# Performance work log

Hardware: AMD Instinct MI355X
Metric: run time of the kernel (lower is better)

The kernel has to match this reference:

```python
import jax, jax.numpy as jnp
import numpy as np

B, T, IN, H, OUT, L = 64, 4096, 32, 128, 32, 2


def setup_inputs() -> dict:
    key = jax.random.key(0)
    ks = jax.random.split(key, 12)
    s = 1.0 / np.sqrt(H)
    inp = {"x": jax.random.normal(ks[0], (B, T, IN), dtype=jnp.float32)}
    # layer 0 (input_dim -> H), layer 1 (H -> H); PyTorch GRU layout: [3H, in] with gates (r, z, n)
    inp["W_ih0"] = jax.random.uniform(ks[1], (3 * H, IN), jnp.float32, -s, s)
    inp["W_hh0"] = jax.random.uniform(ks[2], (3 * H, H), jnp.float32, -s, s)
    inp["b_ih0"] = jax.random.uniform(ks[3], (3 * H,), jnp.float32, -s, s)
    inp["b_hh0"] = jax.random.uniform(ks[4], (3 * H,), jnp.float32, -s, s)
    inp["W_ih1"] = jax.random.uniform(ks[5], (3 * H, H), jnp.float32, -s, s)
    inp["W_hh1"] = jax.random.uniform(ks[6], (3 * H, H), jnp.float32, -s, s)
    inp["b_ih1"] = jax.random.uniform(ks[7], (3 * H,), jnp.float32, -s, s)
    inp["b_hh1"] = jax.random.uniform(ks[8], (3 * H,), jnp.float32, -s, s)
    inp["fc_w"] = jax.random.uniform(ks[9], (OUT, H), jnp.float32, -s, s)
    inp["fc_b"] = jax.random.uniform(ks[10], (OUT,), jnp.float32, -s, s)
    return inp


def _gru_layer(x_seq, W_ih, W_hh, b_ih, b_hh):
    # x_seq: [B, T, in]; precompute the input projection as one big GEMM
    gi = jnp.einsum("bti,gi->btg", x_seq, W_ih) + b_ih  # [B, T, 3H]
    h0 = jnp.zeros((x_seq.shape[0], W_hh.shape[1]), x_seq.dtype)

    def step(h, gi_t):
        gh = h @ W_hh.T + b_hh  # [B, 3H]
        i_r, i_z, i_n = jnp.split(gi_t, 3, axis=-1)
        h_r, h_z, h_n = jnp.split(gh, 3, axis=-1)
        r = jax.nn.sigmoid(i_r + h_r)
        z = jax.nn.sigmoid(i_z + h_z)
        n = jnp.tanh(i_n + r * h_n)
        h_new = (1.0 - z) * n + z * h
        return h_new, h_new

    hT, outs = jax.lax.scan(step, h0, jnp.swapaxes(gi, 0, 1))  # outs: [T, B, H]
    return jnp.swapaxes(outs, 0, 1), hT


def reference(x, W_ih0, W_hh0, b_ih0, b_hh0, W_ih1, W_hh1, b_ih1, b_hh1, fc_w, fc_b):
    y0, h0 = _gru_layer(x, W_ih0, W_hh0, b_ih0, b_hh0)
    y1, h1 = _gru_layer(y0, W_ih1, W_hh1, b_ih1, b_hh1)
    out = jnp.einsum("bth,oh->bto", y1, fc_w) + fc_b  # [B, T, OUT]
    h = jnp.stack([h0, h1], axis=0)  # [n_layers, B, H]
    return out, h
```

## Files before the change

kernel.cpp:

```cpp
#include <hip/hip_runtime.h>

#define BB 64
#define TT 4096
#define IN0 32
#define HH 128
#define NOUT 32

typedef _Float16 h2 __attribute__((ext_vector_type(2)));
typedef _Float16 h8v __attribute__((ext_vector_type(8)));
typedef float f32x4 __attribute__((ext_vector_type(4)));
union H8 { h8v v; h2 p[4]; };

struct SM {
    alignas(16) _Float16 hf0[2][HH];
    alignas(16) _Float16 hf1[2][HH];
    alignas(16) _Float16 xh[2][16][IN0];
    alignas(16) float    pfc[2][NOUT * 20];
    alignas(16) float    outbuf[32][NOUT];
};

__device__ __forceinline__ float fast_sigmoid(float x) {
    x = fminf(fmaxf(x, -30.f), 30.f);
    float e = __expf(-x);
    return __builtin_amdgcn_rcpf(1.f + e);
}
__device__ __forceinline__ float fast_tanh(float x) {
    x = fminf(fmaxf(x, -15.f), 15.f);
    float e = __expf(-2.f * x);
    return (1.f - e) * __builtin_amdgcn_rcpf(1.f + e);
}
__device__ __forceinline__ float fdot2(h2 a, h2 b, float c) {
#if __has_builtin(__builtin_amdgcn_fdot2)
    return __builtin_amdgcn_fdot2(a, b, c, false);
#else
    return fmaf((float)a.x, (float)b.x, fmaf((float)a.y, (float)b.y, c));
#endif
}
__device__ __forceinline__ h2 cvt2(float a, float b) {
    h2 r; r.x = (_Float16)a; r.y = (_Float16)b; return r;
}
__device__ __forceinline__ f32x4 MF(h8v a, h8v b, f32x4 c) {
    return __builtin_amdgcn_mfma_f32_16x16x32_f16(a, b, c, 0, 0, 0);
}

extern "C" __global__ __launch_bounds__(512)
__attribute__((amdgpu_waves_per_eu(2, 2)))
void gru_mfma_kernel(
    const float* __restrict__ x,
    const float* __restrict__ W_ih0, const float* __restrict__ W_hh0,
    const float* __restrict__ b_ih0, const float* __restrict__ b_hh0,
    const float* __restrict__ W_ih1, const float* __restrict__ W_hh1,
    const float* __restrict__ b_ih1, const float* __restrict__ b_hh1,
    const float* __restrict__ fc_w, const float* __restrict__ fc_b,
    float* __restrict__ out, float* __restrict__ hstack)
{
    __shared__ SM sm;
    const int b = blockIdx.x;
    const int tid = threadIdx.x;
    const int w = tid >> 6;
    const int l = tid & 63;
    const int ln = l & 15;
    const int kg = (l >> 4) * 8;
    const int jw = 16 * w + ln;
    const int o = tid & 31, ks = tid >> 5;
    const float* xb = x + (size_t)b * TT * IN0;
    float* outb = out + (size_t)b * TT * NOUT;
    float* hstack_l0 = hstack + (size_t)b * HH;
    float* hstack_l1 = hstack + (size_t)(BB + b) * HH;

    auto LDB = [&](const float* W, int ldk, int row, int kb) -> h8v {
        const float* p = W + (size_t)row * ldk + kb + kg;
        float4 f0 = *(const float4*)p;
        float4 f1 = *(const float4*)(p + 4);
        H8 u;
        u.p[0] = cvt2(f0.x, f0.y); u.p[1] = cvt2(f0.z, f0.w);
        u.p[2] = cvt2(f1.x, f1.y); u.p[3] = cvt2(f1.z, f1.w);
        return u.v;
    };
    h8v Br1i[4], Br1h[4], Bz1i[4], Bz1h[4], Bn1i[4], Bn1h[4];
    h8v Br0[4], Bz0[4], Bh0[4];
    #pragma unroll
    for (int c = 0; c < 4; ++c) {
        Br1i[c] = LDB(W_ih1, HH, jw,       32 * c);
        Bz1i[c] = LDB(W_ih1, HH, jw + 128, 32 * c);
        Bn1i[c] = LDB(W_ih1, HH, jw + 256, 32 * c);
        Br1h[c] = LDB(W_hh1, HH, jw,       32 * c);
        Bz1h[c] = LDB(W_hh1, HH, jw + 128, 32 * c);
        Bn1h[c] = LDB(W_hh1, HH, jw + 256, 32 * c);
        Br0[c]  = LDB(W_hh0, HH, jw,       32 * c);
        Bz0[c]  = LDB(W_hh0, HH, jw + 128, 32 * c);
        Bh0[c]  = LDB(W_hh0, HH, jw + 256, 32 * c);
    }
    const h8v Br0x = LDB(W_ih0, IN0, jw,       0);
    const h8v Bz0x = LDB(W_ih0, IN0, jw + 128, 0);
    const h8v Bn0x = LDB(W_ih0, IN0, jw + 256, 0);

    const float bvr1 = b_ih1[jw] + b_hh1[jw];
    const float bvz1 = b_ih1[jw + 128] + b_hh1[jw + 128];
    const float bvi1 = b_ih1[jw + 256];
    const float bvh1 = b_hh1[jw + 256];
    const float bvr0 = b_ih0[jw] + b_hh0[jw];
    const float bvz0 = b_ih0[jw + 128] + b_hh0[jw + 128];
    const float bvi0 = b_ih0[jw + 256];
    const float bvh0 = b_hh0[jw + 256];
    h2 wfc[4];
    #pragma unroll
    for (int m = 0; m < 4; ++m) {
        float2 f = *(const float2*)&fc_w[(size_t)o * HH + ks * 8 + 2 * m];
        wfc[m] = cvt2(f.x, f.y);
    }
    const float fcbr = fc_b[o];
    const f32x4 z4 = {0.f, 0.f, 0.f, 0.f};

    if (tid < HH) {
        sm.hf0[0][tid] = (_Float16)0.f; sm.hf0[1][tid] = (_Float16)0.f;
        sm.hf1[0][tid] = (_Float16)0.f; sm.hf1[1][tid] = (_Float16)0.f;
    }
    if (tid < 128) {
        float4 f = ((const float4*)xb)[tid];
        ((h2*)&sm.xh[0][0][0])[2 * tid]     = cvt2(f.x, f.y);
        ((h2*)&sm.xh[0][0][0])[2 * tid + 1] = cvt2(f.z, f.w);
    }
    __syncthreads();

    float hp0 = 0.f, hp1 = 0.f;
    float4 pf;
    for (int s = 0; s <= TT + 4; ++s) {
        const int cur = s & 1, nxt = cur ^ 1;
        if (tid < 128 && (s & 15) == 0 && s + 16 < TT)
            pf = ((const float4*)(xb + (size_t)(s + 16) * IN0))[tid];
        if (tid >= 128 && tid < 256 && (s & 15) == 4 && s >= 20 && (s >> 4) <= 256) {
            const int k = tid - 128;
            const int fb = ((s >> 4) - 1) * 16;
            const int t = fb + (k >> 3);
            float4 v = *(const float4*)&sm.outbuf[t & 31][(k & 7) * 4];
            *(float4*)&outb[(size_t)t * NOUT + (k & 7) * 4] = v;
        }
        const _Float16* h0b = &sm.hf0[cur][0] + kg;
        const _Float16* h1b = &sm.hf1[cur][0] + kg;
        const _Float16* xr  = &sm.xh[(s >> 4) & 1][s & 15][0] + kg;
        h8v a0 = *(const h8v*)(h0b);
        h8v a1 = *(const h8v*)(h1b);
        f32x4 r1  = MF(a0, Br1i[0], z4); r1 = MF(a1, Br1h[0], r1);
        f32x4 zz1 = MF(a0, Bz1i[0], z4); zz1 = MF(a1, Bz1h[0], zz1);
        f32x4 n1i = MF(a0, Bn1i[0], z4);
        f32x4 n1h = MF(a1, Bn1h[0], z4);
        f32x4 r0  = MF(a0, Br0[0], z4);
        f32x4 zz0 = MF(a0, Bz0[0], z4);
        f32x4 n0h = MF(a0, Bh0[0], z4);
        #pragma unroll
        for (int c = 1; c < 4; ++c) {
            a0 = *(const h8v*)(h0b + 32 * c);
            a1 = *(const h8v*)(h1b + 32 * c);
            r1  = MF(a0, Br1i[c], r1);  r1  = MF(a1, Br1h[c], r1);
            zz1 = MF(a0, Bz1i[c], zz1); zz1 = MF(a1, Bz1h[c], zz1);
            n1i = MF(a0, Bn1i[c], n1i);
            n1h = MF(a1, Bn1h[c], n1h);
            r0  = MF(a0, Br0[c], r0);
            zz0 = MF(a0, Bz0[c], zz0);
            n0h = MF(a0, Bh0[c], n0h);
        }
        h8v ax = *(const h8v*)xr;
        r0  = MF(ax, Br0x, r0);
        zz0 = MF(ax, Bz0x, zz0);
        f32x4 n0i = MF(ax, Bn0x, z4);

        {
            float rg = fast_sigmoid(r0.x + bvr0);
            float zg = fast_sigmoid(zz0.x + bvz0);
            float ng = fast_tanh(n0i.x + bvi0 + rg * (n0h.x + bvh0));
            float hn = (1.f - zg) * ng + zg * hp0;
            if (s <= TT - 1) {
                hp0 = hn;
                if (l < 16) {
                    sm.hf0[nxt][jw] = (_Float16)hn;
                    if (s == TT - 1) hstack_l0[jw] = hn;
                }
            }
        }
        {
            float rg = fast_sigmoid(r1.x + bvr1);
            float zg = fast_sigmoid(zz1.x + bvz1);
            float ng = fast_tanh(n1i.x + bvi1 + rg * (n1h.x + bvh1));
            float hn = (1.f - zg) * ng + zg * hp1;
            if (s >= 1 && s <= TT) {
                hp1 = hn;
                if (l < 16) {
                    sm.hf1[nxt][jw] = (_Float16)hn;
                    if (s == TT) hstack_l1[jw] = hn;
                }
            }
        }
        if (s >= 2 && s <= TT + 1) {
            H8 hv; hv.v = *(const h8v*)&sm.hf1[cur][ks * 8];
            float ssum = 0.f;
            #pragma unroll
            for (int m = 0; m < 4; ++m) ssum = fdot2(wfc[m], hv.p[m], ssum);
            sm.pfc[cur][o * 20 + ks] = ssum;
        }
        if (s >= 3 && s <= TT + 2 && tid < NOUT) {
            float ssum = fcbr;
            #pragma unroll
            for (int m = 0; m < 4; ++m) {
                float4 v = *(const float4*)&sm.pfc[nxt][tid * 20 + 4 * m];
                ssum += v.x + v.y + v.z + v.w;
            }
            sm.outbuf[(s - 3) & 31][tid] = ssum;
        }
        if (tid < 128 && (s & 15) == 8 && s + 8 < TT) {
            const int buf = ((s >> 4) + 1) & 1;
            ((h2*)&sm.xh[buf][0][0])[2 * tid]     = cvt2(pf.x, pf.y);
            ((h2*)&sm.xh[buf][0][0])[2 * tid + 1] = cvt2(pf.z, pf.w);
        }
        __syncthreads();
    }
}

extern "C" void kernel_launch(void* const* d_in, const int* in_sizes, int n_in,
                              void* d_out, int out_size, void* d_ws, size_t ws_size,
                              hipStream_t stream) {
    const float* x     = (const float*)d_in[0];
    const float* W_ih0 = (const float*)d_in[1];
    const float* W_hh0 = (const float*)d_in[2];
    const float* b_ih0 = (const float*)d_in[3];
    const float* b_hh0 = (const float*)d_in[4];
    const float* W_ih1 = (const float*)d_in[5];
    const float* W_hh1 = (const float*)d_in[6];
    const float* b_ih1 = (const float*)d_in[7];
    const float* b_hh1 = (const float*)d_in[8];
    const float* fc_w  = (const float*)d_in[9];
    const float* fc_b  = (const float*)d_in[10];

    float* out    = (float*)d_out;
    float* hstack = out + (size_t)BB * TT * NOUT;

    gru_mfma_kernel<<<BB, 512, 0, stream>>>(
        x, W_ih0, W_hh0, b_ih0, b_hh0,
        W_ih1, W_hh1, b_ih1, b_hh1,
        fc_w, fc_b, out, hstack);
}
```

Measured before the change: 4.330 ms.

## Compute FC projection with MFMA and unroll time loop by two

Replaces the per-thread fdot2 FC partial sums (16 partials per output) with one MFMA per wave over a 32-wide K chunk, cutting the reduction to 4 partials per output. All h-vector LDS loads are hoisted ahead of the MFMA chain, and the time loop is unrolled by two so the double-buffer index is a compile-time constant. This shortens the serial per-step critical path at the cost of extra registers for the preloaded operands and the FC weight fragment. The loop runs to TT+5 iterations in pairs, so one extra step executes, but the existing guards keep it harmless.

```diff
diff --git a/kernel.cpp b/kernel.cpp
--- a/kernel.cpp
+++ b/kernel.cpp
@@ -28,13 +28,6 @@
     x = fminf(fmaxf(x, -15.f), 15.f);
     float e = __expf(-2.f * x);
     return (1.f - e) * __builtin_amdgcn_rcpf(1.f + e);
-}
-__device__ __forceinline__ float fdot2(h2 a, h2 b, float c) {
-#if __has_builtin(__builtin_amdgcn_fdot2)
-    return __builtin_amdgcn_fdot2(a, b, c, false);
-#else
-    return fmaf((float)a.x, (float)b.x, fmaf((float)a.y, (float)b.y, c));
-#endif
 }
 __device__ __forceinline__ h2 cvt2(float a, float b) {
     h2 r; r.x = (_Float16)a; r.y = (_Float16)b; return r;
@@ -62,7 +55,9 @@
     const int ln = l & 15;
     const int kg = (l >> 4) * 8;
     const int jw = 16 * w + ln;
-    const int o = tid & 31, ks = tid >> 5;
+    const int ofc = 16 * (w & 1) + ln;
+    const int cfc = w >> 1;
+    const int fco = kg + 32 * cfc;
     const float* xb = x + (size_t)b * TT * IN0;
     float* outb = out + (size_t)b * TT * NOUT;
     float* hstack_l0 = hstack + (size_t)b * HH;
@@ -94,6 +89,7 @@
     const h8v Br0x = LDB(W_ih0, IN0, jw,       0);
     const h8v Bz0x = LDB(W_ih0, IN0, jw + 128, 0);
     const h8v Bn0x = LDB(W_ih0, IN0, jw + 256, 0);
+    const h8v Bfc  = LDB(fc_w,  HH,  ofc,      32 * cfc);
 
     const float bvr1 = b_ih1[jw] + b_hh1[jw];
     const float bvz1 = b_ih1[jw + 128] + b_hh1[jw + 128];
@@ -103,13 +99,7 @@
     const float bvz0 = b_ih0[jw + 128] + b_hh0[jw + 128];
     const float bvi0 = b_ih0[jw + 256];
     const float bvh0 = b_hh0[jw + 256];
-    h2 wfc[4];
-    #pragma unroll
-    for (int m = 0; m < 4; ++m) {
-        float2 f = *(const float2*)&fc_w[(size_t)o * HH + ks * 8 + 2 * m];
-        wfc[m] = cvt2(f.x, f.y);
-    }
-    const float fcbr = fc_b[o];
+    const float fcbr = (tid < NOUT) ? fc_b[tid] : 0.f;
     const f32x4 z4 = {0.f, 0.f, 0.f, 0.f};
 
     if (tid < HH) {
@@ -125,8 +115,9 @@
 
     float hp0 = 0.f, hp1 = 0.f;
     float4 pf;
-    for (int s = 0; s <= TT + 4; ++s) {
-        const int cur = s & 1, nxt = cur ^ 1;
+
+    auto body = [&](int s, int cur) {
+        const int nxt = cur ^ 1;
         if (tid < 128 && (s & 15) == 0 && s + 16 < TT)
             pf = ((const float4*)(xb + (size_t)(s + 16) * IN0))[tid];
         if (tid >= 128 && tid < 256 && (s & 15) == 4 && s >= 20 && (s >> 4) <= 256) {
@@ -138,29 +129,32 @@
         }
         const _Float16* h0b = &sm.hf0[cur][0] + kg;
         const _Float16* h1b = &sm.hf1[cur][0] + kg;
-        const _Float16* xr  = &sm.xh[(s >> 4) & 1][s & 15][0] + kg;
-        h8v a0 = *(const h8v*)(h0b);
-        h8v a1 = *(const h8v*)(h1b);
-        f32x4 r1  = MF(a0, Br1i[0], z4); r1 = MF(a1, Br1h[0], r1);
-        f32x4 zz1 = MF(a0, Bz1i[0], z4); zz1 = MF(a1, Bz1h[0], zz1);
-        f32x4 n1i = MF(a0, Bn1i[0], z4);
-        f32x4 n1h = MF(a1, Bn1h[0], z4);
-        f32x4 r0  = MF(a0, Br0[0], z4);
-        f32x4 zz0 = MF(a0, Bz0[0], z4);
-        f32x4 n0h = MF(a0, Bh0[0], z4);
+        h8v a0[4], a1[4];
+        #pragma unroll
+        for (int c = 0; c < 4; ++c) {
+            a0[c] = *(const h8v*)(h0b + 32 * c);
+            a1[c] = *(const h8v*)(h1b + 32 * c);
+        }
+        h8v ax  = *(const h8v*)(&sm.xh[(s >> 4) & 1][s & 15][0] + kg);
+        h8v afc = *(const h8v*)(&sm.hf1[cur][0] + fco);
+        f32x4 r1  = MF(a0[0], Br1i[0], z4); r1  = MF(a1[0], Br1h[0], r1);
+        f32x4 zz1 = MF(a0[0], Bz1i[0], z4); zz1 = MF(a1[0], Bz1h[0], zz1);
+        f32x4 n1i = MF(a0[0], Bn1i[0], z4);
+        f32x4 n1h = MF(a1[0], Bn1h[0], z4);
+        f32x4 r0  = MF(a0[0], Br0[0], z4);
+        f32x4 zz0 = MF(a0[0], Bz0[0], z4);
+        f32x4 n0h = MF(a0[0], Bh0[0], z4);
+        f32x4 pacc = MF(afc, Bfc, z4);
         #pragma unroll
         for (int c = 1; c < 4; ++c) {
-            a0 = *(const h8v*)(h0b + 32 * c);
-            a1 = *(const h8v*)(h1b + 32 * c);
-            r1  = MF(a0, Br1i[c], r1);  r1  = MF(a1, Br1h[c], r1);
-            zz1 = MF(a0, Bz1i[c], zz1); zz1 = MF(a1, Bz1h[c], zz1);
-            n1i = MF(a0, Bn1i[c], n1i);
-            n1h = MF(a1, Bn1h[c], n1h);
-            r0  = MF(a0, Br0[c], r0);
-            zz0 = MF(a0, Bz0[c], zz0);
-            n0h = MF(a0, Bh0[c], n0h);
-        }
-        h8v ax = *(const h8v*)xr;
+            r1  = MF(a0[c], Br1i[c], r1);  r1  = MF(a1[c], Br1h[c], r1);
+            zz1 = MF(a0[c], Bz1i[c], zz1); zz1 = MF(a1[c], Bz1h[c], zz1);
+            n1i = MF(a0[c], Bn1i[c], n1i);
+            n1h = MF(a1[c], Bn1h[c], n1h);
+            r0  = MF(a0[c], Br0[c], r0);
+            zz0 = MF(a0[c], Bz0[c], zz0);
+            n0h = MF(a0[c], Bh0[c], n0h);
+        }
         r0  = MF(ax, Br0x, r0);
         zz0 = MF(ax, Bz0x, zz0);
         f32x4 n0i = MF(ax, Bn0x, z4);
@@ -191,20 +185,14 @@
                 }
             }
         }
-        if (s >= 2 && s <= TT + 1) {
-            H8 hv; hv.v = *(const h8v*)&sm.hf1[cur][ks * 8];
-            float ssum = 0.f;
-            #pragma unroll
-            for (int m = 0; m < 4; ++m) ssum = fdot2(wfc[m], hv.p[m], ssum);
-            sm.pfc[cur][o * 20 + ks] = ssum;
-        }
+        if (s >= 2 && s <= TT + 1 && l < 16)
+            sm.pfc[cur][ofc * 20 + cfc] = pacc.x;
         if (s >= 3 && s <= TT + 2 && tid < NOUT) {
             float ssum = fcbr;
-            #pragma unroll
-            for (int m = 0; m < 4; ++m) {
-                float4 v = *(const float4*)&sm.pfc[nxt][tid * 20 + 4 * m];
-                ssum += v.x + v.y + v.z + v.w;
-            }
+            ssum += sm.pfc[nxt][tid * 20 + 0];
+            ssum += sm.pfc[nxt][tid * 20 + 1];
+            ssum += sm.pfc[nxt][tid * 20 + 2];
+            ssum += sm.pfc[nxt][tid * 20 + 3];
             sm.outbuf[(s - 3) & 31][tid] = ssum;
         }
         if (tid < 128 && (s & 15) == 8 && s + 8 < TT) {
@@ -213,6 +201,11 @@
             ((h2*)&sm.xh[buf][0][0])[2 * tid + 1] = cvt2(pf.z, pf.w);
         }
         __syncthreads();
+    };
+
+    for (int s2 = 0; s2 <= TT + 4; s2 += 2) {
+        body(s2, 0);
+        body(s2 + 1, 1);
     }
 }
 
```

Result: faster. 4.045 ms (-6.6%).
